# Kernel tuning notes

Measured on AMD Instinct MI355X. Metric: run time of the kernel, lower is better.

Reference implementation:

```python
import jax, jax.numpy as jnp
import numpy as np

B, S, D, H = 2, 2048, 1024, 16
DK = D // H

def setup_inputs() -> dict:
    key = jax.random.key(0)
    ks = jax.random.split(key, 5)
    std = 1.0 / np.sqrt(D)
    return {
        "x": jax.random.normal(ks[0], (B, S, D), dtype=jnp.float32),
        "wq": jax.random.normal(ks[1], (D, D), dtype=jnp.float32) * std,
        "wk": jax.random.normal(ks[2], (D, D), dtype=jnp.float32) * std,
        "wv": jax.random.normal(ks[3], (D, D), dtype=jnp.float32) * std,
        "wo": jax.random.normal(ks[4], (D, D), dtype=jnp.float32) * std,
    }

def reference(x, wq, wk, wv, wo):
    b, s, d = x.shape
    # torch Linear(bias=False): x @ W.T
    q = (x @ wq.T).reshape(b, s, H, DK).transpose(0, 2, 1, 3)  # [b,h,s,dk]
    k = (x @ wk.T).reshape(b, s, H, DK).transpose(0, 2, 1, 3)
    v = (x @ wv.T).reshape(b, s, H, DK).transpose(0, 2, 1, 3)
    scale = jnp.sqrt(jnp.asarray(DK, dtype=x.dtype))
    scores = jnp.einsum('bhqd,bhkd->bhqk', q, k) / scale  # [b,h,s,s]
    # causal mask (masking=True): lower-triangular kept, rest -inf
    causal = jnp.tril(jnp.ones((s, s), dtype=bool))
    scores = jnp.where(causal[None, None], scores, -jnp.inf)
    attn = jax.nn.softmax(scores, axis=-1)
    out = jnp.einsum('bhqk,bhkd->bhqd', attn, v)  # [b,h,s,dk]
    out = out.transpose(0, 2, 1, 3).reshape(b, s, d)
    return out @ wo.T
```

## Files before the change

### kernel.cpp

```cpp
#include <hip/hip_runtime.h>

#define LB __launch_bounds__(256)

typedef __bf16 bf16x8 __attribute__((ext_vector_type(8)));
typedef float f32x4 __attribute__((ext_vector_type(4)));
typedef float f32x16 __attribute__((ext_vector_type(16)));
typedef unsigned int u32;
typedef unsigned int u32x2 __attribute__((ext_vector_type(2)));

constexpr int B = 2, S = 2048, D = 1024, H = 16, DK = 64;
constexpr int M = B * S;
constexpr int K = D;

__device__ __forceinline__ unsigned short f2bf(float f) {
    union { float f; unsigned u; } v; v.f = f;
    unsigned r = v.u + 0x7fffu + ((v.u >> 16) & 1u);
    return (unsigned short)(r >> 16);
}

__device__ __forceinline__ u32 pk2bf(float lo, float hi) {
    union { __bf16 h[2]; u32 w; } u;
    u.h[0] = (__bf16)lo; u.h[1] = (__bf16)hi;
    return u.w;
}

__device__ __forceinline__ float fexp2(float x) {
    float y;
    asm("v_exp_f32 %0, %1" : "=v"(y) : "v"(x));
    return y;
}

__device__ __forceinline__ void gld_lds16(const unsigned short* g, unsigned short* l) {
    __builtin_amdgcn_global_load_lds(
        (const __attribute__((address_space(1))) unsigned int*)g,
        (__attribute__((address_space(3))) unsigned int*)l, 16, 0, 0);
}

__global__ LB void cvt_all(const float* __restrict__ x,  const float* __restrict__ wq,
                           const float* __restrict__ wk, const float* __restrict__ wv,
                           const float* __restrict__ wo, unsigned short* __restrict__ dst) {
    const size_t NX = (size_t)M * D;
    const size_t NW = (size_t)D * D;
    size_t i = ((size_t)blockIdx.x * 256 + threadIdx.x) * 4;
    if (i >= NX + 4 * NW) return;
    const float* src; size_t off;
    if      (i < NX)          { src = x;  off = i; }
    else if (i < NX + NW)     { src = wq; off = i - NX; }
    else if (i < NX + 2 * NW) { src = wk; off = i - NX - NW; }
    else if (i < NX + 3 * NW) { src = wv; off = i - NX - 2 * NW; }
    else                      { src = wo; off = i - NX - 3 * NW; }
    float4 f = *reinterpret_cast<const float4*>(src + off);
    ushort4 o;
    o.x = f2bf(f.x); o.y = f2bf(f.y); o.z = f2bf(f.z); o.w = f2bf(f.w);
    *reinterpret_cast<ushort4*>(dst + i) = o;
}

__global__ LB void gemm_qkv(const unsigned short* __restrict__ A,
                            const unsigned short* __restrict__ wqb,
                            const unsigned short* __restrict__ wkb,
                            const unsigned short* __restrict__ wvb,
                            unsigned short* __restrict__ qo,
                            unsigned short* __restrict__ ko,
                            unsigned short* __restrict__ vo) {
    __shared__ __align__(16) unsigned short lA[128 * 32];
    __shared__ __align__(16) unsigned short lB[128 * 32];
    const int z = blockIdx.y;
    const unsigned short* W = (z == 0) ? wqb : ((z == 1) ? wkb : wvb);
    int bid = blockIdx.x;
    int m0 = (((bid >> 6) << 3) | (bid & 7)) * 128;
    int n0 = ((bid >> 3) & 7) * 128;
    int t = threadIdx.x;
    int w = t >> 6, lane = t & 63;
    int r = lane & 15, g = lane >> 4;
    int wr = w >> 1, wc = w & 1;
    int rowT = t >> 2, colOff = (t & 3) * 8;

    f32x4 acc[4][4];
#pragma unroll
    for (int mi = 0; mi < 4; ++mi)
#pragma unroll
        for (int ni = 0; ni < 4; ++ni) acc[mi][ni] = f32x4{0.f, 0.f, 0.f, 0.f};

    for (int k0 = 0; k0 < K; k0 += 32) {
        gld_lds16(A + (size_t)(m0 + rowT) * K + k0 + colOff,      lA + (w * 64) * 8);
        gld_lds16(A + (size_t)(m0 + 64 + rowT) * K + k0 + colOff, lA + (256 + w * 64) * 8);
        gld_lds16(W + (size_t)(n0 + rowT) * K + k0 + colOff,      lB + (w * 64) * 8);
        gld_lds16(W + (size_t)(n0 + 64 + rowT) * K + k0 + colOff, lB + (256 + w * 64) * 8);
        __syncthreads();
        bf16x8 af[4], bfr[4];
#pragma unroll
        for (int mi = 0; mi < 4; ++mi)
            af[mi] = *reinterpret_cast<const bf16x8*>(&lA[(wr * 64 + mi * 16 + r) * 32 + g * 8]);
#pragma unroll
        for (int ni = 0; ni < 4; ++ni)
            bfr[ni] = *reinterpret_cast<const bf16x8*>(&lB[(wc * 64 + ni * 16 + r) * 32 + g * 8]);
#pragma unroll
        for (int mi = 0; mi < 4; ++mi)
#pragma unroll
            for (int ni = 0; ni < 4; ++ni)
                acc[mi][ni] = __builtin_amdgcn_mfma_f32_16x16x32_bf16(af[mi], bfr[ni], acc[mi][ni], 0, 0, 0);
        __syncthreads();
    }

    const float QSCALE = 0.125f * 1.44269504088896341f;
    float scale = (z == 0) ? QSCALE : 1.0f;
    unsigned short* dst = (z == 0) ? qo : ((z == 1) ? ko : vo);
#pragma unroll
    for (int mi = 0; mi < 4; ++mi)
#pragma unroll
        for (int ni = 0; ni < 4; ++ni)
#pragma unroll
            for (int j = 0; j < 4; ++j) {
                int row = m0 + wr * 64 + mi * 16 + g * 4 + j;
                int col = n0 + wc * 64 + ni * 16 + r;
                int b = row >> 11, s = row & (S - 1);
                int h = col >> 6, dk = col & 63;
                size_t bh = (size_t)(b * H + h);
                unsigned short val = f2bf(acc[mi][ni][j] * scale);
                if (z == 0) {
                    dst[(bh * S + s) * DK + dk] = val;
                } else if (z == 1) {
                    int kt32 = s >> 5, q5k = s & 31;
                    int dsi = dk >> 4, hlk = (dk >> 3) & 1, e = dk & 7;
                    dst[(((bh * 64 + kt32) * 4 + dsi) * 64 + (hlk * 32 + q5k)) * 8 + e] = val;
                } else {
                    int ktile = s >> 6, ks2 = (s >> 4) & 3, hlv = (s >> 3) & 1, e = s & 7;
                    int rh = dk >> 5, q5r = dk & 31;
                    dst[(((bh * 32 + ktile) * 8 + rh * 4 + ks2) * 64 + (hlv * 32 + q5r)) * 8 + e] = val;
                }
            }
}

__global__ LB void out_gemm(const unsigned short* __restrict__ A,
                            const unsigned short* __restrict__ W,
                            float* __restrict__ out) {
    __shared__ __align__(16) unsigned short lA[128 * 32];
    __shared__ __align__(16) unsigned short lB[64 * 32];
    int bid = blockIdx.x;
    int m0 = (((bid >> 7) << 3) | (bid & 7)) * 128;
    int n0 = ((bid >> 3) & 15) * 64;
    int t = threadIdx.x;
    int w = t >> 6, lane = t & 63;
    int r = lane & 15, g = lane >> 4;
    int wr = w >> 1, wc = w & 1;
    int rowT = t >> 2, colOff = (t & 3) * 8;

    f32x4 acc[4][2];
#pragma unroll
    for (int mi = 0; mi < 4; ++mi)
#pragma unroll
        for (int ni = 0; ni < 2; ++ni) acc[mi][ni] = f32x4{0.f, 0.f, 0.f, 0.f};

    for (int k0 = 0; k0 < K; k0 += 32) {
        gld_lds16(A + (size_t)(m0 + rowT) * K + k0 + colOff,      lA + (w * 64) * 8);
        gld_lds16(A + (size_t)(m0 + 64 + rowT) * K + k0 + colOff, lA + (256 + w * 64) * 8);
        gld_lds16(W + (size_t)(n0 + rowT) * K + k0 + colOff,      lB + (w * 64) * 8);
        __syncthreads();
        bf16x8 af[4], bfr[2];
#pragma unroll
        for (int mi = 0; mi < 4; ++mi)
            af[mi] = *reinterpret_cast<const bf16x8*>(&lA[(wr * 64 + mi * 16 + r) * 32 + g * 8]);
#pragma unroll
        for (int ni = 0; ni < 2; ++ni)
            bfr[ni] = *reinterpret_cast<const bf16x8*>(&lB[(wc * 32 + ni * 16 + r) * 32 + g * 8]);
#pragma unroll
        for (int mi = 0; mi < 4; ++mi)
#pragma unroll
            for (int ni = 0; ni < 2; ++ni)
                acc[mi][ni] = __builtin_amdgcn_mfma_f32_16x16x32_bf16(af[mi], bfr[ni], acc[mi][ni], 0, 0, 0);
        __syncthreads();
    }

#pragma unroll
    for (int mi = 0; mi < 4; ++mi)
#pragma unroll
        for (int ni = 0; ni < 2; ++ni)
#pragma unroll
            for (int j = 0; j < 4; ++j) {
                int row = m0 + wr * 64 + mi * 16 + g * 4 + j;
                int col = n0 + wc * 32 + ni * 16 + r;
                out[(size_t)row * D + col] = acc[mi][ni][j];
            }
}

__global__ __launch_bounds__(64) void flash_attn(
        const unsigned short* __restrict__ q,
        const unsigned short* __restrict__ kmat,
        const unsigned short* __restrict__ vt,
        unsigned short* __restrict__ ao) {
    int bid = blockIdx.x;
    int kk = bid >> 8, cc = bid & 255;
    int r9 = (kk << 8) | ((kk & 1) ? (255 - cc) : cc);
    int qt = 63 - (r9 >> 5);
    int bh = r9 & 31;
    int b = bh >> 4, hd = bh & 15;
    int q0 = qt << 5;
    int nt = (qt + 2) >> 1;

    int l = threadIdx.x;
    int q5 = l & 31, hl = l >> 5;
    int qglob = q0 + q5;

    const unsigned short* qp = q    + (size_t)bh * S * DK;
    const unsigned short* kf = kmat + (size_t)bh * S * DK;
    const unsigned short* vf = vt   + (size_t)bh * S * DK;

    bf16x8 ones;
#pragma unroll
    for (int i = 0; i < 8; ++i) ones[i] = (__bf16)1.0f;

    const f32x16 z16 = {0,0,0,0,0,0,0,0,0,0,0,0,0,0,0,0};

    bf16x8 qf[4];
#pragma unroll
    for (int dsi = 0; dsi < 4; ++dsi)
        qf[dsi] = *reinterpret_cast<const bf16x8*>(qp + (size_t)qglob * DK + dsi * 16 + hl * 8);

    f32x16 acc0 = z16, acc1 = z16, accl = z16;

    auto loadK = [&](bf16x8 (&kr)[8], int kb) {
        const unsigned short* base = kf + (size_t)(kb >> 5) * 4 * 512 + l * 8;
#pragma unroll
        for (int dsi = 0; dsi < 4; ++dsi) {
            kr[dsi]     = *reinterpret_cast<const bf16x8*>(base + dsi * 512);
            kr[4 + dsi] = *reinterpret_cast<const bf16x8*>(base + (4 + dsi) * 512);
        }
    };
    auto loadV = [&](bf16x8 (&vr)[8], int kb) {
        const unsigned short* base = vf + (size_t)(kb >> 6) * 8 * 512 + l * 8;
#pragma unroll
        for (int i2 = 0; i2 < 8; ++i2)
            vr[i2] = *reinterpret_cast<const bf16x8*>(base + i2 * 512);
    };
    auto compute = [&](bf16x8 (&kr)[8], bf16x8 (&vr)[8], int kb) {
        f32x16 st0 = __builtin_amdgcn_mfma_f32_32x32x16_bf16(kr[0], qf[0], z16, 0, 0, 0);
        f32x16 st1 = __builtin_amdgcn_mfma_f32_32x32x16_bf16(kr[4], qf[0], z16, 0, 0, 0);
#pragma unroll
        for (int dsi = 1; dsi < 4; ++dsi) {
            st0 = __builtin_amdgcn_mfma_f32_32x32x16_bf16(kr[dsi],     qf[dsi], st0, 0, 0, 0);
            st1 = __builtin_amdgcn_mfma_f32_32x32x16_bf16(kr[4 + dsi], qf[dsi], st1, 0, 0, 0);
        }
        if (kb + 31 > q0) {
#pragma unroll
            for (int r = 0; r < 16; ++r) {
                int kv = kb + (r & 3) + 8 * (r >> 2) + 4 * hl;
                st0[r] = (kv <= qglob) ? st0[r] : -1e30f;
            }
        }
        if (kb + 63 > q0) {
#pragma unroll
            for (int r = 0; r < 16; ++r) {
                int kv = kb + 32 + (r & 3) + 8 * (r >> 2) + 4 * hl;
                st1[r] = (kv <= qglob) ? st1[r] : -1e30f;
            }
        }
#pragma unroll
        for (int r = 0; r < 16; ++r) { st0[r] = fexp2(st0[r]); st1[r] = fexp2(st1[r]); }
        u32 pk[2][8];
#pragma unroll
        for (int rg = 0; rg < 4; ++rg) {
            pk[0][2*rg]   = pk2bf(st0[4*rg],   st0[4*rg+1]);
            pk[0][2*rg+1] = pk2bf(st0[4*rg+2], st0[4*rg+3]);
            pk[1][2*rg]   = pk2bf(st1[4*rg],   st1[4*rg+1]);
            pk[1][2*rg+1] = pk2bf(st1[4*rg+2], st1[4*rg+3]);
        }
        union PF { bf16x8 vv; u32 w[4]; } pf[4];
#pragma unroll
        for (int ti2 = 0; ti2 < 2; ++ti2)
#pragma unroll
            for (int s = 0; s < 2; ++s) {
                u32x2 r0 = __builtin_amdgcn_permlane32_swap(pk[ti2][4*s],   pk[ti2][4*s+2], false, false);
                u32x2 r1 = __builtin_amdgcn_permlane32_swap(pk[ti2][4*s+1], pk[ti2][4*s+3], false, false);
                PF f;
                f.w[0] = r0[0]; f.w[1] = r1[0];
                f.w[2] = r0[1]; f.w[3] = r1[1];
                pf[ti2*2+s] = f;
            }
#pragma unroll
        for (int ks = 0; ks < 4; ++ks) {
            acc0 = __builtin_amdgcn_mfma_f32_32x32x16_bf16(vr[ks],     pf[ks].vv, acc0, 0, 0, 0);
            acc1 = __builtin_amdgcn_mfma_f32_32x32x16_bf16(vr[4 + ks], pf[ks].vv, acc1, 0, 0, 0);
            accl = __builtin_amdgcn_mfma_f32_32x32x16_bf16(ones,       pf[ks].vv, accl, 0, 0, 0);
        }
    };

    bf16x8 ka[8], kb2[8], va[8], vb2[8];
    loadK(ka, 0);
    loadV(va, 0);
    int it = 0;
    while (true) {
        if (it + 1 < nt) { loadK(kb2, (it + 1) << 6); loadV(vb2, (it + 1) << 6); }
        compute(ka, va, it << 6);
        ++it; if (it >= nt) break;
        if (it + 1 < nt) { loadK(ka, (it + 1) << 6); loadV(va, (it + 1) << 6); }
        compute(kb2, vb2, it << 6);
        ++it; if (it >= nt) break;
    }

    float inv = 1.0f / accl[0];
    size_t obase = ((size_t)(b * S + qglob)) * D + hd * DK;
#pragma unroll
    for (int rg = 0; rg < 4; ++rg) {
        uint2 wd;
        wd.x = pk2bf(acc0[4*rg]   * inv, acc0[4*rg+1] * inv);
        wd.y = pk2bf(acc0[4*rg+2] * inv, acc0[4*rg+3] * inv);
        *reinterpret_cast<uint2*>(ao + obase + rg * 8 + hl * 4) = wd;
        uint2 we;
        we.x = pk2bf(acc1[4*rg]   * inv, acc1[4*rg+1] * inv);
        we.y = pk2bf(acc1[4*rg+2] * inv, acc1[4*rg+3] * inv);
        *reinterpret_cast<uint2*>(ao + obase + 32 + rg * 8 + hl * 4) = we;
    }
}

extern "C" void kernel_launch(void* const* d_in, const int* in_sizes, int n_in,
                              void* d_out, int out_size, void* d_ws, size_t ws_size,
                              hipStream_t stream) {
    const float* x  = (const float*)d_in[0];
    const float* wq = (const float*)d_in[1];
    const float* wk = (const float*)d_in[2];
    const float* wv = (const float*)d_in[3];
    const float* wo = (const float*)d_in[4];
    char* ws = (char*)d_ws;
    unsigned short* xb  = (unsigned short*)(ws);
    unsigned short* wqb = (unsigned short*)(ws + (size_t)(8  << 20));
    unsigned short* wkb = (unsigned short*)(ws + (size_t)(10 << 20));
    unsigned short* wvb = (unsigned short*)(ws + (size_t)(12 << 20));
    unsigned short* wob = (unsigned short*)(ws + (size_t)(14 << 20));
    unsigned short* qb  = (unsigned short*)(ws + (size_t)(16 << 20));
    unsigned short* kb  = (unsigned short*)(ws + (size_t)(24 << 20));
    unsigned short* vtb = (unsigned short*)(ws + (size_t)(32 << 20));
    unsigned short* aob = (unsigned short*)(ws + (size_t)(40 << 20));

    cvt_all<<<8192, 256, 0, stream>>>(x, wq, wk, wv, wo, xb);

    gemm_qkv<<<dim3(256, 3), 256, 0, stream>>>(xb, wqb, wkb, wvb, qb, kb, vtb);
    flash_attn<<<2048, 64, 0, stream>>>(qb, kb, vtb, aob);
    out_gemm<<<512, 256, 0, stream>>>(aob, wob, (float*)d_out);
}
```

Baseline: 104.9 us.

## Software-pipeline QK^T of next tile with softmax and PV of current tile

Restructures the attention inner loop so the QK^T MFMAs for tile it+1 are issued before the exp/mask/PV work for tile it. K and V now use single register buffers, with K prefetched two tiles ahead and V loaded after the current PV. The aim is to overlap matrix-core work with the VALU exp and permute work and to cut register use from the double-buffered K/V. The risk is that the single V buffer exposes V load latency, since each V load is issued right before the PV step that consumes it.

```diff
diff --git a/kernel.cpp b/kernel.cpp
--- a/kernel.cpp
+++ b/kernel.cpp
@@ -218,7 +218,8 @@
 
     f32x16 acc0 = z16, acc1 = z16, accl = z16;
 
-    auto loadK = [&](bf16x8 (&kr)[8], int kb) {
+    bf16x8 kr[8], vr[8];
+    auto loadK = [&](int kb) {
         const unsigned short* base = kf + (size_t)(kb >> 5) * 4 * 512 + l * 8;
 #pragma unroll
         for (int dsi = 0; dsi < 4; ++dsi) {
@@ -226,20 +227,22 @@
             kr[4 + dsi] = *reinterpret_cast<const bf16x8*>(base + (4 + dsi) * 512);
         }
     };
-    auto loadV = [&](bf16x8 (&vr)[8], int kb) {
+    auto loadV = [&](int kb) {
         const unsigned short* base = vf + (size_t)(kb >> 6) * 8 * 512 + l * 8;
 #pragma unroll
         for (int i2 = 0; i2 < 8; ++i2)
             vr[i2] = *reinterpret_cast<const bf16x8*>(base + i2 * 512);
     };
-    auto compute = [&](bf16x8 (&kr)[8], bf16x8 (&vr)[8], int kb) {
-        f32x16 st0 = __builtin_amdgcn_mfma_f32_32x32x16_bf16(kr[0], qf[0], z16, 0, 0, 0);
-        f32x16 st1 = __builtin_amdgcn_mfma_f32_32x32x16_bf16(kr[4], qf[0], z16, 0, 0, 0);
+    auto qkRaw = [&](f32x16& s0, f32x16& s1) {
+        s0 = __builtin_amdgcn_mfma_f32_32x32x16_bf16(kr[0], qf[0], z16, 0, 0, 0);
+        s1 = __builtin_amdgcn_mfma_f32_32x32x16_bf16(kr[4], qf[0], z16, 0, 0, 0);
 #pragma unroll
         for (int dsi = 1; dsi < 4; ++dsi) {
-            st0 = __builtin_amdgcn_mfma_f32_32x32x16_bf16(kr[dsi],     qf[dsi], st0, 0, 0, 0);
-            st1 = __builtin_amdgcn_mfma_f32_32x32x16_bf16(kr[4 + dsi], qf[dsi], st1, 0, 0, 0);
-        }
+            s0 = __builtin_amdgcn_mfma_f32_32x32x16_bf16(kr[dsi],     qf[dsi], s0, 0, 0, 0);
+            s1 = __builtin_amdgcn_mfma_f32_32x32x16_bf16(kr[4 + dsi], qf[dsi], s1, 0, 0, 0);
+        }
+    };
+    auto finish = [&](f32x16& st0, f32x16& st1, int kb) {
         if (kb + 31 > q0) {
 #pragma unroll
             for (int r = 0; r < 16; ++r) {
@@ -284,16 +287,24 @@
         }
     };
 
-    bf16x8 ka[8], kb2[8], va[8], vb2[8];
-    loadK(ka, 0);
-    loadV(va, 0);
+    f32x16 sA0, sA1, sB0, sB1;
+
+    loadK(0);
+    loadV(0);
+    qkRaw(sA0, sA1);
+    if (nt > 1) loadK(64);
+
     int it = 0;
     while (true) {
-        if (it + 1 < nt) { loadK(kb2, (it + 1) << 6); loadV(vb2, (it + 1) << 6); }
-        compute(ka, va, it << 6);
+        if (it + 1 < nt) qkRaw(sB0, sB1);
+        if (it + 2 < nt) loadK((it + 2) << 6);
+        finish(sA0, sA1, it << 6);
+        if (it + 1 < nt) loadV((it + 1) << 6);
         ++it; if (it >= nt) break;
-        if (it + 1 < nt) { loadK(ka, (it + 1) << 6); loadV(va, (it + 1) << 6); }
-        compute(kb2, vb2, it << 6);
+        if (it + 1 < nt) qkRaw(sA0, sA1);
+        if (it + 2 < nt) loadK((it + 2) << 6);
+        finish(sB0, sB1, it << 6);
+        if (it + 1 < nt) loadV((it + 1) << 6);
         ++it; if (it >= nt) break;
     }
 
```

Result: no change. 105.6 us (+0.7%).
